# Kernel optimization log

Measured on AMD Instinct MI355X. Metric: run time of the kernel, lower is better.

Reference implementation:

```python
import jax, jax.numpy as jnp
import numpy as np

EPS = 1.0
SIGMA = 1.0
N = 4096

def setup_inputs() -> dict:
    key = jax.random.key(0)
    k1, k2 = jax.random.split(key)
    q = jax.random.uniform(k1, (N, 3), dtype=jnp.float32) * 5.0
    p = jax.random.normal(k2, (N, 3), dtype=jnp.float32) * 0.1
    m = jnp.ones((N, 1), dtype=jnp.float32)
    return {"q": q, "p": p, "m": m, "t": 0}

def reference(q, p, m, t):
    # all-pairs displacement: disp[i, j] = q[i] - q[j], shape [N, N, 3]
    disp = q[:, None, :] - q[None, :, :]
    r = jnp.linalg.norm(disp, axis=2)  # [N, N]
    n = q.shape[0]
    eye = jnp.eye(n, dtype=bool)
    r = jnp.where(eye, 1.0, r)  # fill_diagonal_(1) to avoid div-by-zero

    prefix = 48.0 * EPS
    sigma12 = SIGMA ** 12
    sigma6 = SIGMA ** 6
    inner = sigma12 / r ** 13 - 0.5 * sigma6 / r ** 7
    inner = jnp.where(eye, 0.0, inner)  # fill_diagonal_(0)
    direction = disp / r[:, :, None]
    force = -prefix * inner[:, :, None] * direction  # [N, N, 3]

    dq = p / m
    dp = force.sum(axis=1)  # [N, 3]
    return (dq, dp)
```

## Files before the change

kernel.cpp:

```cpp
#include <hip/hip_runtime.h>

#define N 4096
#define BLOCK 256
#define JC 64
#define JCHUNK (N / JC)

template <bool DIAG>
__device__ __forceinline__ void lj_accum(const float* __restrict__ qj, int j0, int i,
                                         float qx, float qy, float qz,
                                         float& fx, float& fy, float& fz) {
    #pragma unroll 8
    for (int jj = 0; jj < JCHUNK; ++jj) {
        const float dx = qx - qj[jj * 3 + 0];
        const float dy = qy - qj[jj * 3 + 1];
        const float dz = qz - qj[jj * 3 + 2];
        const float r2 = fmaf(dx, dx, fmaf(dy, dy, dz * dz));
        const float inv_r2 = __builtin_amdgcn_rcpf(r2);
        const float inv_r4 = inv_r2 * inv_r2;
        const float inv_r6 = inv_r4 * inv_r2;
        const float inv_r8 = inv_r4 * inv_r4;
        float s = inv_r8 * fmaf(-48.0f, inv_r6, 24.0f);
        if (DIAG) s = (j0 + jj == i) ? 0.0f : s;
        fx = fmaf(s, dx, fx);
        fy = fmaf(s, dy, fy);
        fz = fmaf(s, dz, fz);
    }
}

__global__ __launch_bounds__(BLOCK)
void lj_partial_kernel(const float* __restrict__ q, float* __restrict__ ws) {
    const int bx  = blockIdx.x;
    const int by  = blockIdx.y;
    const int i   = bx * BLOCK + threadIdx.x;
    const int j0  = by * JCHUNK;
    const float* __restrict__ qj = q + j0 * 3;

    const float qx = q[i*3+0], qy = q[i*3+1], qz = q[i*3+2];
    float fx = 0.f, fy = 0.f, fz = 0.f;

    if ((by >> 2) == bx)
        lj_accum<true >(qj, j0, i, qx, qy, qz, fx, fy, fz);
    else
        lj_accum<false>(qj, j0, i, qx, qy, qz, fx, fy, fz);

    float* w = ws + (size_t)by * 3 * N;
    w[0*N + i] = fx;
    w[1*N + i] = fy;
    w[2*N + i] = fz;
}

__global__ __launch_bounds__(BLOCK)
void lj_reduce_kernel(const float* __restrict__ ws, const float* __restrict__ p,
                      const float* __restrict__ m, float* __restrict__ out) {
    const int u = blockIdx.x * BLOCK + threadIdx.x;
    out[u] = p[u] / m[u / 3];
    const int c = u >> 12;
    const int i = u & (N - 1);
    float acc = 0.f;
    #pragma unroll 8
    for (int k = 0; k < JC; ++k)
        acc += ws[((size_t)k * 3 + c) * N + i];
    out[N*3 + i*3 + c] = acc;
}

extern "C" void kernel_launch(void* const* d_in, const int* in_sizes, int n_in,
                              void* d_out, int out_size, void* d_ws, size_t ws_size,
                              hipStream_t stream) {
    const float* q = (const float*)d_in[0];
    const float* p = (const float*)d_in[1];
    const float* m = (const float*)d_in[2];
    float* out = (float*)d_out;
    float* ws  = (float*)d_ws;

    dim3 gridA(N / BLOCK, JC);
    lj_partial_kernel<<<gridA, BLOCK, 0, stream>>>(q, ws);

    lj_reduce_kernel<<<(N * 3) / BLOCK, BLOCK, 0, stream>>>(ws, p, m, out);
}
```

Before: 16.11 us.

## Process two i-particles per thread with packed v2f math and move dq into partial kernel

Each thread now handles two i-particles using 2-wide float vectors, so every j-position load is reused across two interactions and the compiler can emit packed FMA/mul instructions. The grid halves in x (512 i per block), and the diagonal-block test is adjusted to match. The dq = p/m computation moves from the reduce kernel into the partial kernel's first j-chunk blocks. The cost is more registers per thread and half as many blocks, which lowers parallelism on a grid that was already small.

```diff
diff --git a/kernel.cpp b/kernel.cpp
--- a/kernel.cpp
+++ b/kernel.cpp
@@ -2,58 +2,86 @@
 
 #define N 4096
 #define BLOCK 256
+#define IBLK 512
 #define JC 64
 #define JCHUNK (N / JC)
 
+typedef float v2f __attribute__((ext_vector_type(2)));
+
 template <bool DIAG>
-__device__ __forceinline__ void lj_accum(const float* __restrict__ qj, int j0, int i,
-                                         float qx, float qy, float qz,
-                                         float& fx, float& fy, float& fz) {
+__device__ __forceinline__ void lj_accum2(const float* __restrict__ qj, int j0,
+                                          int ia, int ib,
+                                          v2f qx2, v2f qy2, v2f qz2,
+                                          v2f& fx2, v2f& fy2, v2f& fz2) {
+    const v2f C24  = {24.0f, 24.0f};
+    const v2f Cm48 = {-48.0f, -48.0f};
     #pragma unroll 8
     for (int jj = 0; jj < JCHUNK; ++jj) {
-        const float dx = qx - qj[jj * 3 + 0];
-        const float dy = qy - qj[jj * 3 + 1];
-        const float dz = qz - qj[jj * 3 + 2];
-        const float r2 = fmaf(dx, dx, fmaf(dy, dy, dz * dz));
-        const float inv_r2 = __builtin_amdgcn_rcpf(r2);
-        const float inv_r4 = inv_r2 * inv_r2;
-        const float inv_r6 = inv_r4 * inv_r2;
-        const float inv_r8 = inv_r4 * inv_r4;
-        float s = inv_r8 * fmaf(-48.0f, inv_r6, 24.0f);
-        if (DIAG) s = (j0 + jj == i) ? 0.0f : s;
-        fx = fmaf(s, dx, fx);
-        fy = fmaf(s, dy, fy);
-        fz = fmaf(s, dz, fz);
+        const float jx = qj[jj*3+0];
+        const float jy = qj[jj*3+1];
+        const float jz = qj[jj*3+2];
+        v2f dx = qx2 - jx;
+        v2f dy = qy2 - jy;
+        v2f dz = qz2 - jz;
+        v2f r2 = __builtin_elementwise_fma(dx, dx,
+                 __builtin_elementwise_fma(dy, dy, dz * dz));
+        v2f u;
+        u.x = __builtin_amdgcn_rcpf(r2.x);
+        u.y = __builtin_amdgcn_rcpf(r2.y);
+        v2f u2 = u * u;
+        v2f u3 = u2 * u;
+        v2f u4 = u2 * u2;
+        v2f s = u4 * __builtin_elementwise_fma(Cm48, u3, C24);
+        if (DIAG) {
+            const int j = j0 + jj;
+            s.x = (j == ia) ? 0.0f : s.x;
+            s.y = (j == ib) ? 0.0f : s.y;
+        }
+        fx2 = __builtin_elementwise_fma(s, dx, fx2);
+        fy2 = __builtin_elementwise_fma(s, dy, fy2);
+        fz2 = __builtin_elementwise_fma(s, dz, fz2);
     }
 }
 
 __global__ __launch_bounds__(BLOCK)
-void lj_partial_kernel(const float* __restrict__ q, float* __restrict__ ws) {
-    const int bx  = blockIdx.x;
-    const int by  = blockIdx.y;
-    const int i   = bx * BLOCK + threadIdx.x;
-    const int j0  = by * JCHUNK;
+void lj_partial_kernel(const float* __restrict__ q, const float* __restrict__ p,
+                       const float* __restrict__ m, float* __restrict__ out,
+                       float* __restrict__ ws) {
+    const int bx = blockIdx.x;
+    const int by = blockIdx.y;
+    const int ia = bx * IBLK + threadIdx.x;
+    const int ib = ia + BLOCK;
+    const int j0 = by * JCHUNK;
     const float* __restrict__ qj = q + j0 * 3;
 
-    const float qx = q[i*3+0], qy = q[i*3+1], qz = q[i*3+2];
-    float fx = 0.f, fy = 0.f, fz = 0.f;
+    const v2f qx2 = {q[ia*3+0], q[ib*3+0]};
+    const v2f qy2 = {q[ia*3+1], q[ib*3+1]};
+    const v2f qz2 = {q[ia*3+2], q[ib*3+2]};
+    v2f fx2 = {0.f, 0.f}, fy2 = {0.f, 0.f}, fz2 = {0.f, 0.f};
 
-    if ((by >> 2) == bx)
-        lj_accum<true >(qj, j0, i, qx, qy, qz, fx, fy, fz);
+    if ((by >> 3) == bx)
+        lj_accum2<true >(qj, j0, ia, ib, qx2, qy2, qz2, fx2, fy2, fz2);
     else
-        lj_accum<false>(qj, j0, i, qx, qy, qz, fx, fy, fz);
+        lj_accum2<false>(qj, j0, ia, ib, qx2, qy2, qz2, fx2, fy2, fz2);
 
     float* w = ws + (size_t)by * 3 * N;
-    w[0*N + i] = fx;
-    w[1*N + i] = fy;
-    w[2*N + i] = fz;
+    w[0*N + ia] = fx2.x;  w[0*N + ib] = fx2.y;
+    w[1*N + ia] = fy2.x;  w[1*N + ib] = fy2.y;
+    w[2*N + ia] = fz2.x;  w[2*N + ib] = fz2.y;
+
+    if (by == 0) {
+        const int base = bx * (IBLK * 3);
+        #pragma unroll
+        for (int k = 0; k < (IBLK * 3) / BLOCK; ++k) {
+            const int t = base + k * BLOCK + threadIdx.x;
+            out[t] = p[t] / m[t / 3];
+        }
+    }
 }
 
 __global__ __launch_bounds__(BLOCK)
-void lj_reduce_kernel(const float* __restrict__ ws, const float* __restrict__ p,
-                      const float* __restrict__ m, float* __restrict__ out) {
+void lj_reduce_kernel(const float* __restrict__ ws, float* __restrict__ out) {
     const int u = blockIdx.x * BLOCK + threadIdx.x;
-    out[u] = p[u] / m[u / 3];
     const int c = u >> 12;
     const int i = u & (N - 1);
     float acc = 0.f;
@@ -72,8 +100,8 @@
     float* out = (float*)d_out;
     float* ws  = (float*)d_ws;
 
-    dim3 gridA(N / BLOCK, JC);
-    lj_partial_kernel<<<gridA, BLOCK, 0, stream>>>(q, ws);
+    dim3 gridA(N / IBLK, JC);
+    lj_partial_kernel<<<gridA, BLOCK, 0, stream>>>(q, p, m, out, ws);
 
-    lj_reduce_kernel<<<(N * 3) / BLOCK, BLOCK, 0, stream>>>(ws, p, m, out);
+    lj_reduce_kernel<<<(N * 3) / BLOCK, BLOCK, 0, stream>>>(ws, out);
 }
```

Result: slower. 17.37 us (+7.9%).
